# Kernel tuning notes

Hardware: AMD Instinct MI355X
Metric: run time of the kernel (lower is better)

Reference implementation:

```python
import jax, jax.numpy as jnp
import numpy as np

B, N, D, E, H, HS = 2, 1024, 256, 64, 8, 64
FF = 4 * D
EPS = 1e-6


def _glorot(key, shape):
    fan_in, fan_out = shape[-2], shape[-1]
    lim = np.sqrt(6.0 / (fan_in + fan_out))
    return jax.random.uniform(key, shape, jnp.float32, -lim, lim)


def setup_inputs() -> dict:
    key = jax.random.key(0)
    ks = jax.random.split(key, 10)
    return {
        "node": jax.random.normal(ks[0], (B, N, D), jnp.float32),
        "edge": jax.random.normal(ks[1], (B, N, N, E), jnp.float32),
        "Wq": _glorot(ks[2], (H, D, HS)),
        "Wk": _glorot(ks[3], (H, D + E, HS)),
        "Wv": _glorot(ks[4], (H, D, HS)),
        "Wp": _glorot(ks[5], (H, HS, D)),
        "bp": jnp.zeros((D,), jnp.float32),
        "ln1_g": jnp.ones((D,), jnp.float32),
        "ln1_b": jnp.zeros((D,), jnp.float32),
        "W1": _glorot(ks[6], (D, FF)),
        "b1": jnp.zeros((FF,), jnp.float32),
        "W2": _glorot(ks[7], (FF, D)),
        "b2": jnp.zeros((D,), jnp.float32),
        "ln2_g": jnp.ones((D,), jnp.float32),
        "ln2_b": jnp.zeros((D,), jnp.float32),
    }


def _layernorm(x, g, b):
    mu = jnp.mean(x, axis=-1, keepdims=True)
    var = jnp.mean(jnp.square(x - mu), axis=-1, keepdims=True)
    return (x - mu) * jax.lax.rsqrt(var + EPS) * g + b


def reference(node, edge, Wq, Wk, Wv, Wp, bp, ln1_g, ln1_b, W1, b1, W2, b2, ln2_g, ln2_b):
    d_in = node.shape[-1]
    head_size = Wq.shape[-1]
    # query projection, scaled by sqrt(head_size)
    q = jnp.einsum('bni,hio->bnho', node, Wq) / jnp.sqrt(jnp.asarray(head_size, node.dtype))
    # key kernel split: node part [H, D, HS] and edge part [H, E, HS].
    # concat([repeat(key), edge]) @ Wk  ==  key @ Wk[:, :D] + edge @ Wk[:, D:]
    kn = jnp.einsum('bmi,hio->bmho', node, Wk[:, :d_in])          # [B,M,H,HS]
    logits = jnp.einsum('bnho,bmho->bhnm', q, kn)                 # node-key logits
    qe = jnp.einsum('bnho,heo->bnhe', q, Wk[:, d_in:])            # [B,N,H,E]
    logits = logits + jnp.einsum('bnhe,bnme->bhnm', qe, edge)     # edge-conditioned logits
    attn = jax.nn.softmax(logits, axis=-1)                        # [B,H,N,M]
    v = jnp.einsum('bmi,hio->bmho', node, Wv)                     # [B,M,H,HS]
    mo = jnp.einsum('bhnm,bmho->bnho', attn, v)                   # [B,N,H,HS]
    mha = jnp.einsum('bnhi,hio->bno', mo, Wp) + bp                # output projection
    # residual + layernorm (dropout = identity at eval)
    x = _layernorm(node + mha, ln1_g, ln1_b)
    # FFN: one hidden layer of ff_multi*D with relu, then project back to D
    ff = jax.nn.relu(x @ W1 + b1) @ W2 + b2
    return _layernorm(x + ff, ln2_g, ln2_b)
```

## Files before the change

### kernel.cpp

```cpp
#include <hip/hip_runtime.h>
#include <hip/hip_bf16.h>
#include <hip/hip_fp16.h>

#define B_  2
#define N_  1024
#define D_  256
#define E_  64
#define H_  8
#define HS_ 64
#define FF_ 1024
#define R_  (B_*N_)

typedef short bf8 __attribute__((ext_vector_type(8)));
typedef float f4  __attribute__((ext_vector_type(4)));

static __device__ __forceinline__ ushort f2b(float f) {
  __hip_bfloat16 h = __float2bfloat16(f);
  return *reinterpret_cast<ushort*>(&h);
}

static __device__ __forceinline__ ushort4 f4_to_b4(float4 v) {
  ushort4 r;
  r.x = f2b(v.x); r.y = f2b(v.y); r.z = f2b(v.z); r.w = f2b(v.w);
  return r;
}

__global__ void k_pack(const float* __restrict__ node, const float* __restrict__ Wq,
                       const float* __restrict__ Wk, const float* __restrict__ Wv,
                       const float* __restrict__ Wp, const float* __restrict__ W1,
                       const float* __restrict__ W2,
                       ushort* __restrict__ node_bf, ushort* __restrict__ wqkvT,
                       ushort* __restrict__ wkeT, ushort* __restrict__ wpT,
                       ushort* __restrict__ w1T, ushort* __restrict__ w2T) {
  int idx = blockIdx.x * 256 + threadIdx.x;
  if (idx < 524288) {
    node_bf[idx] = f2b(node[idx]);
    return;
  }
  idx -= 524288;
  if (idx < 393216) {
    int c = idx >> 8, i = idx & 255;
    int mat = c >> 9, h = (c >> 6) & 7, o = c & 63;
    float v;
    if (mat == 0)      v = Wq[(h * 256 + i) * 64 + o] * 0.125f;
    else if (mat == 1) v = Wk[(h * 320 + i) * 64 + o];
    else               v = Wv[(h * 256 + i) * 64 + o];
    wqkvT[idx] = f2b(v);
    return;
  }
  idx -= 393216;
  if (idx < 262144) {
    int c = idx >> 9, r = idx & 511;
    int h2 = c >> 6, e = c & 63, h = r >> 6, o = r & 63;
    wkeT[idx] = (h2 == h) ? f2b(Wk[(h * 320 + 256 + e) * 64 + o]) : (ushort)0;
    return;
  }
  idx -= 262144;
  if (idx < 131072) {
    int c = idx >> 9, r = idx & 511;
    wpT[idx] = f2b(Wp[r * 256 + c]);
    return;
  }
  idx -= 131072;
  if (idx < 262144) {
    int c = idx >> 8, k = idx & 255;
    w1T[idx] = f2b(W1[k * 1024 + c]);
    return;
  }
  idx -= 262144;
  {
    int c = idx >> 10, k = idx & 1023;
    w2T[idx] = f2b(W2[k * 256 + c]);
  }
}

__global__ void k_vT(const ushort* __restrict__ qkv, ushort* __restrict__ vt) {
  int idx = blockIdx.x * 256 + threadIdx.x;
  if (idx >= 16 * 64 * 1024) return;
  int m = idx & 1023;
  int rest = idx >> 10;
  int o = rest & 63;
  int bh = rest >> 6;
  int b = bh >> 3, h = bh & 7;
  vt[idx] = qkv[(size_t)(b * 1024 + m) * 1536 + 1024 + h * 64 + o];
}

template<int EPI, int OFMT>
__global__ void k_gemm(const ushort* __restrict__ A, const ushort* __restrict__ Bt,
                       void* __restrict__ Cv, const float* __restrict__ bias,
                       int M, int N, int K, int lda, int ldbt, int ldc,
                       long long as1, long long as2, long long bs1, long long bs2,
                       long long cs1, long long cs2) {
  int z = blockIdx.z;
  const ushort* Ab = A  + (size_t)((z >> 3) * as1 + (z & 7) * as2);
  const ushort* Bb = Bt + (size_t)((z >> 3) * bs1 + (z & 7) * bs2);
  size_t coff = (size_t)((z >> 3) * cs1 + (z & 7) * cs2);
  int r0 = blockIdx.x * 64, c0 = blockIdx.y * 64;

  __shared__ ushort As[64][40];
  __shared__ ushort Bs[64][40];

  int tid = threadIdx.x;
  int lane = tid & 63, w = tid >> 6;
  int wm = w >> 1, wn = w & 1;
  int kg = lane >> 4, lr = lane & 15;

  f4 acc[2][2] = {};

  for (int k0 = 0; k0 < K; k0 += 32) {
    __syncthreads();
    {
      int row = tid >> 2, ch = tid & 3;
      *(int4*)&As[row][ch * 8] = *(const int4*)(Ab + (size_t)(r0 + row) * lda + k0 + ch * 8);
    }
    {
      int row = tid >> 2, ch = tid & 3;
      *(int4*)&Bs[row][ch * 8] = *(const int4*)(Bb + (size_t)(c0 + row) * ldbt + k0 + ch * 8);
    }
    __syncthreads();

    bf8 bfr[2];
    #pragma unroll
    for (int cb = 0; cb < 2; ++cb)
      bfr[cb] = *(const bf8*)&Bs[wn * 32 + cb * 16 + lr][kg * 8];
    #pragma unroll
    for (int rb = 0; rb < 2; ++rb) {
      bf8 af = *(const bf8*)&As[wm * 32 + rb * 16 + lr][kg * 8];
      #pragma unroll
      for (int cb = 0; cb < 2; ++cb)
        acc[rb][cb] = __builtin_amdgcn_mfma_f32_16x16x32_bf16(af, bfr[cb], acc[rb][cb], 0, 0, 0);
    }
  }

  float*  Cf = (float*)Cv;
  ushort* Cb = (ushort*)Cv;
  __half* Ch = (__half*)Cv;
  #pragma unroll
  for (int rb = 0; rb < 2; ++rb) {
    #pragma unroll
    for (int cb = 0; cb < 2; ++cb) {
      #pragma unroll
      for (int rr = 0; rr < 4; ++rr) {
        int row = r0 + wm * 32 + rb * 16 + kg * 4 + rr;
        int col = c0 + wn * 32 + cb * 16 + lr;
        size_t ci = coff + (size_t)row * ldc + col;
        float v = acc[rb][cb][rr];
        if (EPI >= 2) v += bias[col];
        if (EPI == 3) v = fmaxf(v, 0.0f);
        if (OFMT == 1)      Cb[ci] = f2b(v);
        else if (OFMT == 2) Ch[ci] = __float2half(v);
        else                Cf[ci] = v;
      }
    }
  }
}

__global__ __launch_bounds__(256, 4) void k_fused(
    const float* __restrict__ edge, const float* __restrict__ qe,
    const __half* __restrict__ logN, ushort* __restrict__ attn) {
  int bid = blockIdx.x;
  int b = bid >> 10, n = bid & 1023;
  int t = threadIdx.x;
  int lane = t & 63, w = t >> 6;
  int kg = lane >> 4, lr = lane & 15;

  __shared__ ushort As[128 * 64];
  __shared__ __half lg[1024 * 9];
  __shared__ float red[2][4][8];

  bf8 bq[2];
  {
    const float* qrow = qe + (size_t)bid * 512 + (size_t)(lr & 7) * 64;
    #pragma unroll
    for (int kk = 0; kk < 2; ++kk) {
      float4 a  = *reinterpret_cast<const float4*>(&qrow[kk * 32 + kg * 8]);
      float4 c4 = *reinterpret_cast<const float4*>(&qrow[kk * 32 + kg * 8 + 4]);
      bq[kk][0] = (short)f2b(a.x);  bq[kk][1] = (short)f2b(a.y);
      bq[kk][2] = (short)f2b(a.z);  bq[kk][3] = (short)f2b(a.w);
      bq[kk][4] = (short)f2b(c4.x); bq[kk][5] = (short)f2b(c4.y);
      bq[kk][6] = (short)f2b(c4.z); bq[kk][7] = (short)f2b(c4.w);
    }
  }

  const float* eb = edge + (size_t)bid * 65536;

  float4 pf[8];
  #pragma unroll
  for (int u = 0; u < 8; ++u)
    pf[u] = reinterpret_cast<const float4*>(eb)[t + 256 * u];

  #pragma unroll 1
  for (int tl = 0; tl < 8; ++tl) {
    __syncthreads();
    #pragma unroll
    for (int u = 0; u < 8; ++u) {
      int g = t + 256 * u;
      int rl = g >> 4, c = t & 15;
      int slot = (c >> 1) ^ (rl & 7), half = c & 1;
      *reinterpret_cast<ushort4*>(&As[rl * 64 + slot * 8 + half * 4]) = f4_to_b4(pf[u]);
    }
    if (tl < 7) {
      const float4* src = reinterpret_cast<const float4*>(eb + (tl + 1) * 8192);
      #pragma unroll
      for (int u = 0; u < 8; ++u) pf[u] = src[t + 256 * u];
    }
    __syncthreads();

    #pragma unroll
    for (int sub = 0; sub < 2; ++sub) {
      int sr = w * 32 + sub * 16 + lr;
      f4 acc = {};
      #pragma unroll
      for (int kk = 0; kk < 2; ++kk) {
        bf8 af = *reinterpret_cast<const bf8*>(&As[sr * 64 + (((kk * 4 + kg) ^ (sr & 7)) << 3)]);
        acc = __builtin_amdgcn_mfma_f32_16x16x32_bf16(af, bq[kk], acc, 0, 0, 0);
      }
      if (lr < 8) {
        int mbase = tl * 128 + w * 32 + sub * 16 + kg * 4;
        #pragma unroll
        for (int rr = 0; rr < 4; ++rr)
          lg[(mbase + rr) * 9 + lr] = __float2half(acc[rr]);
      }
    }
  }
  __syncthreads();

  float l[4][8];
  #pragma unroll
  for (int j = 0; j < 4; ++j) {
    int m = t + 256 * j;
    #pragma unroll
    for (int h = 0; h < 8; ++h)
      l[j][h] = __half2float(lg[m * 9 + h]) +
                __half2float(logN[((size_t)(b * 8 + h) * 1024 + n) * 1024 + m]);
  }
  float mx[8], sm[8];
  #pragma unroll
  for (int h = 0; h < 8; ++h) {
    float v = fmaxf(fmaxf(l[0][h], l[1][h]), fmaxf(l[2][h], l[3][h]));
    #pragma unroll
    for (int off = 32; off; off >>= 1) v = fmaxf(v, __shfl_xor(v, off));
    if (lane == 0) red[0][w][h] = v;
  }
  __syncthreads();
  #pragma unroll
  for (int h = 0; h < 8; ++h)
    mx[h] = fmaxf(fmaxf(red[0][0][h], red[0][1][h]), fmaxf(red[0][2][h], red[0][3][h]));
  #pragma unroll
  for (int j = 0; j < 4; ++j)
    #pragma unroll
    for (int h = 0; h < 8; ++h)
      l[j][h] = __expf(l[j][h] - mx[h]);
  #pragma unroll
  for (int h = 0; h < 8; ++h) {
    float v = l[0][h] + l[1][h] + l[2][h] + l[3][h];
    #pragma unroll
    for (int off = 32; off; off >>= 1) v += __shfl_xor(v, off);
    if (lane == 0) red[1][w][h] = v;
  }
  __syncthreads();
  #pragma unroll
  for (int h = 0; h < 8; ++h)
    sm[h] = 1.0f / (red[1][0][h] + red[1][1][h] + red[1][2][h] + red[1][3][h]);
  #pragma unroll
  for (int h = 0; h < 8; ++h) {
    size_t base = ((size_t)(b * 8 + h) * 1024 + n) * 1024;
    #pragma unroll
    for (int j = 0; j < 4; ++j)
      attn[base + t + 256 * j] = f2b(l[j][h] * sm[h]);
  }
}

__global__ void k_ln(const float* __restrict__ a, const float* __restrict__ bb,
                     const float* __restrict__ g, const float* __restrict__ be,
                     float* __restrict__ of, ushort* __restrict__ ob) {
  int r = blockIdx.x, i = threadIdx.x;
  float t = a[(size_t)r * 256 + i] + bb[(size_t)r * 256 + i];
  __shared__ float red[4];

  float s = t;
  for (int off = 32; off; off >>= 1) s += __shfl_xor(s, off);
  if ((i & 63) == 0) red[i >> 6] = s;
  __syncthreads();
  float mean = (red[0] + red[1] + red[2] + red[3]) * (1.0f / 256.0f);
  __syncthreads();

  float d = t - mean;
  float q = d * d;
  for (int off = 32; off; off >>= 1) q += __shfl_xor(q, off);
  if ((i & 63) == 0) red[i >> 6] = q;
  __syncthreads();
  float var = (red[0] + red[1] + red[2] + red[3]) * (1.0f / 256.0f);

  float y = d * rsqrtf(var + 1e-6f) * g[i] + be[i];
  of[(size_t)r * 256 + i] = y;
  if (ob) ob[(size_t)r * 256 + i] = f2b(y);
}


extern "C" void kernel_launch(void* const* d_in, const int* in_sizes, int n_in,
                              void* d_out, int out_size, void* d_ws, size_t ws_size,
                              hipStream_t stream) {
  (void)in_sizes; (void)n_in; (void)out_size; (void)ws_size;
  const float* node = (const float*)d_in[0];
  const float* edge = (const float*)d_in[1];
  const float* Wq   = (const float*)d_in[2];
  const float* Wk   = (const float*)d_in[3];
  const float* Wv   = (const float*)d_in[4];
  const float* Wp   = (const float*)d_in[5];
  const float* bp   = (const float*)d_in[6];
  const float* g1   = (const float*)d_in[7];
  const float* be1  = (const float*)d_in[8];
  const float* W1   = (const float*)d_in[9];
  const float* b1   = (const float*)d_in[10];
  const float* W2   = (const float*)d_in[11];
  const float* b2   = (const float*)d_in[12];
  const float* g2   = (const float*)d_in[13];
  const float* be2  = (const float*)d_in[14];
  float* out = (float*)d_out;

  char* ws = (char*)d_ws;
  size_t off = 0;
  auto alloc = [&](size_t bytes) -> char* {
    char* p = ws + off;
    off = (off + bytes + 255) & ~(size_t)255;
    return p;
  };
  ushort* node_bf = (ushort*)alloc((size_t)R_ * D_ * 2);
  ushort* wqkvT   = (ushort*)alloc((size_t)1536 * 256 * 2);
  ushort* wkeT    = (ushort*)alloc((size_t)512 * 512 * 2);
  ushort* wpT     = (ushort*)alloc((size_t)256 * 512 * 2);
  ushort* w1T     = (ushort*)alloc((size_t)1024 * 256 * 2);
  ushort* w2T     = (ushort*)alloc((size_t)256 * 1024 * 2);
  ushort* qkv     = (ushort*)alloc((size_t)R_ * 1536 * 2);
  float*  qe      = (float*) alloc((size_t)R_ * 512 * 4);
  ushort* vt      = (ushort*)alloc((size_t)16 * 64 * 1024 * 2);
  __half* logits  = (__half*)alloc((size_t)16 * 1024 * 1024 * 2);
  ushort* attn    = (ushort*)alloc((size_t)16 * 1024 * 1024 * 2);
  ushort* mo      = (ushort*)alloc((size_t)R_ * 512 * 2);
  float*  mha     = (float*) alloc((size_t)R_ * 256 * 4);
  float*  xf      = (float*) alloc((size_t)R_ * 256 * 4);
  ushort* xb      = (ushort*)alloc((size_t)R_ * 256 * 2);
  ushort* hb      = (ushort*)alloc((size_t)R_ * 1024 * 2);
  float*  ff      = (float*) alloc((size_t)R_ * 256 * 4);

  k_pack<<<dim3(7168), dim3(256), 0, stream>>>(node, Wq, Wk, Wv, Wp, W1, W2,
                                               node_bf, wqkvT, wkeT, wpT, w1T, w2T);

  k_gemm<0, 1><<<dim3(32, 24, 1), dim3(256), 0, stream>>>(
      node_bf, wqkvT, qkv, nullptr, 2048, 1536, 256, 256, 256, 1536,
      0LL, 0LL, 0LL, 0LL, 0LL, 0LL);

  k_gemm<0, 0><<<dim3(32, 8, 1), dim3(256), 0, stream>>>(
      qkv, wkeT, qe, nullptr, 2048, 512, 512, 1536, 512, 512,
      0LL, 0LL, 0LL, 0LL, 0LL, 0LL);

  k_vT<<<dim3(4096), dim3(256), 0, stream>>>(qkv, vt);

  k_gemm<0, 2><<<dim3(16, 16, 16), dim3(256), 0, stream>>>(
      qkv, qkv + 512, logits, nullptr, 1024, 1024, 64, 1536, 1536, 1024,
      1572864LL, 64LL, 1572864LL, 64LL, 8388608LL, 1048576LL);

  k_fused<<<dim3(2048), dim3(256), 0, stream>>>(edge, qe, logits, attn);

  k_gemm<0, 1><<<dim3(16, 1, 16), dim3(256), 0, stream>>>(
      attn, vt, mo, nullptr, 1024, 64, 1024, 1024, 1024, 512,
      8388608LL, 1048576LL, 524288LL, 65536LL, 524288LL, 64LL);

  k_gemm<2, 0><<<dim3(32, 4, 1), dim3(256), 0, stream>>>(
      mo, wpT, mha, bp, 2048, 256, 512, 512, 512, 256,
      0LL, 0LL, 0LL, 0LL, 0LL, 0LL);

  k_ln<<<dim3(2048), dim3(256), 0, stream>>>(node, mha, g1, be1, xf, xb);

  k_gemm<3, 1><<<dim3(32, 16, 1), dim3(256), 0, stream>>>(
      xb, w1T, hb, b1, 2048, 1024, 256, 256, 256, 1024,
      0LL, 0LL, 0LL, 0LL, 0LL, 0LL);

  k_gemm<2, 0><<<dim3(32, 4, 1), dim3(256), 0, stream>>>(
      hb, w2T, ff, b2, 2048, 256, 1024, 1024, 1024, 256,
      0LL, 0LL, 0LL, 0LL, 0LL, 0LL);

  k_ln<<<dim3(2048), dim3(256), 0, stream>>>(xf, ff, g2, be2, out, nullptr);
}
```

Before: 231.6 us.

## Widen logits GEMM tile, skip zero blocks in qe GEMM, prefetch logN

The GEMM kernel gains an NBT template parameter so one block can cover several 64-column tiles. The node-logits GEMM uses four tiles per block, which reuses the A tile and launches fewer blocks. A BDIAG mode limits the K loop of the qe GEMM to the diagonal 64-wide slice, because the edge-key weight matrix is block-diagonal per head, so the multiplications by zero are skipped. In the fused softmax kernel, the fp16 node logits are now loaded into registers before the barrier so their global-load latency overlaps the shared-memory wait, at the cost of higher register pressure.

New measurement: 226.8 us. -2.1%, faster.

```diff
diff --git a/kernel.cpp b/kernel.cpp
--- a/kernel.cpp
+++ b/kernel.cpp
@@ -85,7 +85,7 @@
   vt[idx] = qkv[(size_t)(b * 1024 + m) * 1536 + 1024 + h * 64 + o];
 }
 
-template<int EPI, int OFMT>
+template<int EPI, int OFMT, int NBT, bool BDIAG>
 __global__ void k_gemm(const ushort* __restrict__ A, const ushort* __restrict__ Bt,
                        void* __restrict__ Cv, const float* __restrict__ bias,
                        int M, int N, int K, int lda, int ldbt, int ldc,
@@ -95,40 +95,45 @@
   const ushort* Ab = A  + (size_t)((z >> 3) * as1 + (z & 7) * as2);
   const ushort* Bb = Bt + (size_t)((z >> 3) * bs1 + (z & 7) * bs2);
   size_t coff = (size_t)((z >> 3) * cs1 + (z & 7) * cs2);
-  int r0 = blockIdx.x * 64, c0 = blockIdx.y * 64;
+  int r0 = blockIdx.x * 64, c0 = blockIdx.y * (64 * NBT);
 
   __shared__ ushort As[64][40];
-  __shared__ ushort Bs[64][40];
+  __shared__ ushort Bs[64 * NBT][40];
 
   int tid = threadIdx.x;
   int lane = tid & 63, w = tid >> 6;
   int wm = w >> 1, wn = w & 1;
   int kg = lane >> 4, lr = lane & 15;
 
-  f4 acc[2][2] = {};
-
-  for (int k0 = 0; k0 < K; k0 += 32) {
+  f4 acc[2][2 * NBT] = {};
+
+  int kbeg = BDIAG ? c0 : 0;
+  int kend = BDIAG ? c0 + 64 : K;
+  for (int k0 = kbeg; k0 < kend; k0 += 32) {
     __syncthreads();
     {
       int row = tid >> 2, ch = tid & 3;
       *(int4*)&As[row][ch * 8] = *(const int4*)(Ab + (size_t)(r0 + row) * lda + k0 + ch * 8);
     }
-    {
-      int row = tid >> 2, ch = tid & 3;
+    #pragma unroll
+    for (int i = 0; i < NBT; ++i) {
+      int row = (tid >> 2) + 64 * i, ch = tid & 3;
       *(int4*)&Bs[row][ch * 8] = *(const int4*)(Bb + (size_t)(c0 + row) * ldbt + k0 + ch * 8);
     }
     __syncthreads();
 
-    bf8 bfr[2];
-    #pragma unroll
-    for (int cb = 0; cb < 2; ++cb)
-      bfr[cb] = *(const bf8*)&Bs[wn * 32 + cb * 16 + lr][kg * 8];
+    bf8 bfr[2 * NBT];
+    #pragma unroll
+    for (int nt = 0; nt < NBT; ++nt)
+      #pragma unroll
+      for (int cb = 0; cb < 2; ++cb)
+        bfr[nt * 2 + cb] = *(const bf8*)&Bs[nt * 64 + wn * 32 + cb * 16 + lr][kg * 8];
     #pragma unroll
     for (int rb = 0; rb < 2; ++rb) {
       bf8 af = *(const bf8*)&As[wm * 32 + rb * 16 + lr][kg * 8];
       #pragma unroll
-      for (int cb = 0; cb < 2; ++cb)
-        acc[rb][cb] = __builtin_amdgcn_mfma_f32_16x16x32_bf16(af, bfr[cb], acc[rb][cb], 0, 0, 0);
+      for (int q = 0; q < 2 * NBT; ++q)
+        acc[rb][q] = __builtin_amdgcn_mfma_f32_16x16x32_bf16(af, bfr[q], acc[rb][q], 0, 0, 0);
     }
   }
 
@@ -138,13 +143,13 @@
   #pragma unroll
   for (int rb = 0; rb < 2; ++rb) {
     #pragma unroll
-    for (int cb = 0; cb < 2; ++cb) {
+    for (int q = 0; q < 2 * NBT; ++q) {
       #pragma unroll
       for (int rr = 0; rr < 4; ++rr) {
         int row = r0 + wm * 32 + rb * 16 + kg * 4 + rr;
-        int col = c0 + wn * 32 + cb * 16 + lr;
+        int col = c0 + (q >> 1) * 64 + wn * 32 + (q & 1) * 16 + lr;
         size_t ci = coff + (size_t)row * ldc + col;
-        float v = acc[rb][cb][rr];
+        float v = acc[rb][q][rr];
         if (EPI >= 2) v += bias[col];
         if (EPI == 3) v = fmaxf(v, 0.0f);
         if (OFMT == 1)      Cb[ci] = f2b(v);
@@ -223,6 +228,14 @@
       }
     }
   }
+
+  ushort lNr[4][8];
+  #pragma unroll
+  for (int j = 0; j < 4; ++j)
+    #pragma unroll
+    for (int h = 0; h < 8; ++h)
+      lNr[j][h] = *reinterpret_cast<const ushort*>(
+          &logN[((size_t)(b * 8 + h) * 1024 + n) * 1024 + t + 256 * j]);
   __syncthreads();
 
   float l[4][8];
@@ -232,7 +245,7 @@
     #pragma unroll
     for (int h = 0; h < 8; ++h)
       l[j][h] = __half2float(lg[m * 9 + h]) +
-                __half2float(logN[((size_t)(b * 8 + h) * 1024 + n) * 1024 + m]);
+                __half2float(*reinterpret_cast<const __half*>(&lNr[j][h]));
   }
   float mx[8], sm[8];
   #pragma unroll
@@ -347,37 +360,37 @@
   k_pack<<<dim3(7168), dim3(256), 0, stream>>>(node, Wq, Wk, Wv, Wp, W1, W2,
                                                node_bf, wqkvT, wkeT, wpT, w1T, w2T);
 
-  k_gemm<0, 1><<<dim3(32, 24, 1), dim3(256), 0, stream>>>(
+  k_gemm<0, 1, 1, false><<<dim3(32, 24, 1), dim3(256), 0, stream>>>(
       node_bf, wqkvT, qkv, nullptr, 2048, 1536, 256, 256, 256, 1536,
       0LL, 0LL, 0LL, 0LL, 0LL, 0LL);
 
-  k_gemm<0, 0><<<dim3(32, 8, 1), dim3(256), 0, stream>>>(
+  k_gemm<0, 0, 1, true><<<dim3(32, 8, 1), dim3(256), 0, stream>>>(
       qkv, wkeT, qe, nullptr, 2048, 512, 512, 1536, 512, 512,
       0LL, 0LL, 0LL, 0LL, 0LL, 0LL);
 
   k_vT<<<dim3(4096), dim3(256), 0, stream>>>(qkv, vt);
 
-  k_gemm<0, 2><<<dim3(16, 16, 16), dim3(256), 0, stream>>>(
+  k_gemm<0, 2, 4, false><<<dim3(16, 4, 16), dim3(256), 0, stream>>>(
       qkv, qkv + 512, logits, nullptr, 1024, 1024, 64, 1536, 1536, 1024,
       1572864LL, 64LL, 1572864LL, 64LL, 8388608LL, 1048576LL);
 
   k_fused<<<dim3(2048), dim3(256), 0, stream>>>(edge, qe, logits, attn);
 
-  k_gemm<0, 1><<<dim3(16, 1, 16), dim3(256), 0, stream>>>(
+  k_gemm<0, 1, 1, false><<<dim3(16, 1, 16), dim3(256), 0, stream>>>(
       attn, vt, mo, nullptr, 1024, 64, 1024, 1024, 1024, 512,
       8388608LL, 1048576LL, 524288LL, 65536LL, 524288LL, 64LL);
 
-  k_gemm<2, 0><<<dim3(32, 4, 1), dim3(256), 0, stream>>>(
+  k_gemm<2, 0, 1, false><<<dim3(32, 4, 1), dim3(256), 0, stream>>>(
       mo, wpT, mha, bp, 2048, 256, 512, 512, 512, 256,
       0LL, 0LL, 0LL, 0LL, 0LL, 0LL);
 
   k_ln<<<dim3(2048), dim3(256), 0, stream>>>(node, mha, g1, be1, xf, xb);
 
-  k_gemm<3, 1><<<dim3(32, 16, 1), dim3(256), 0, stream>>>(
+  k_gemm<3, 1, 1, false><<<dim3(32, 16, 1), dim3(256), 0, stream>>>(
       xb, w1T, hb, b1, 2048, 1024, 256, 256, 256, 1024,
       0LL, 0LL, 0LL, 0LL, 0LL, 0LL);
 
-  k_gemm<2, 0><<<dim3(32, 4, 1), dim3(256), 0, stream>>>(
+  k_gemm<2, 0, 1, false><<<dim3(32, 4, 1), dim3(256), 0, stream>>>(
       hb, w2T, ff, b2, 2048, 256, 1024, 1024, 1024, 256,
       0LL, 0LL, 0LL, 0LL, 0LL, 0LL);
 
```
